# Kernel optimization log

Measured on AMD Instinct MI355X. Metric: run time of the kernel, lower is better.

Reference implementation:

```python
import jax, jax.numpy as jnp
import numpy as np

N_NODES = 50000
N_EDGES = 800000
D_IN = 64
D_OUT = 64


def setup_inputs() -> dict:
    key = jax.random.key(0)
    k1, k2, k3, k4 = jax.random.split(key, 4)
    x = jax.random.normal(k1, (N_NODES, D_IN), dtype=jnp.float32)
    edge_index = jax.random.randint(k2, (2, N_EDGES), 0, N_NODES, dtype=jnp.int64)
    W = jax.random.normal(k3, (D_IN, D_OUT), dtype=jnp.float32) * (1.0 / np.sqrt(D_IN))
    b = jax.random.normal(k4, (D_OUT,), dtype=jnp.float32) * 0.01
    return {"x": x, "edge_index": edge_index, "W": W, "b": b}


def reference(x, edge_index, W, b):
    N = x.shape[0]
    # Add self-loops (PyG GCNConv default add_self_loops=True)
    loop = jnp.arange(N, dtype=edge_index.dtype)
    src = jnp.concatenate([edge_index[0], loop])  # source j
    dst = jnp.concatenate([edge_index[1], loop])  # target i
    # Linear transform first (standard GCNConv: theta then propagate)
    xw = x @ W  # [N, D_OUT]
    # Symmetric degree normalization: deg over targets of (A + I)
    ones = jnp.ones(src.shape[0], dtype=x.dtype)
    deg = jax.ops.segment_sum(ones, dst, num_segments=N)
    dis = jnp.where(deg > 0, jax.lax.rsqrt(jnp.maximum(deg, 1.0)), 0.0)
    norm = dis[src] * dis[dst]  # [E+N]
    # Gather, weight, scatter-add
    msgs = norm[:, None] * xw[src]  # [E+N, D_OUT]
    out = jax.ops.segment_sum(msgs, dst, num_segments=N) + b
    return jax.nn.relu(out)
```

## Files before the change

### kernel.cpp

```cpp
#include <hip/hip_runtime.h>

#define N_NODES 50000
#define N_EDGES 800000
#define D 64
#define FINE_SHIFT 6
#define NBUCK 782
#define CAP 1280
#define SEGCAP 64
#define EPB 8192
#define NPART 98
#define NMM 196
#define NSTART (NBUCK + 1)

typedef _Float16 f16;
typedef __attribute__((ext_vector_type(4))) _Float16 f16x4;
typedef __attribute__((ext_vector_type(8))) _Float16 f16x8;
typedef __attribute__((ext_vector_type(4))) float f32x4;

#define SMEM_PART (2 * NBUCK * 4 + EPB * 4)
#define SMEM_MM   (64 * 72 * 2 + 256 * 72 * 2)
#define SMEM_SZ   (SMEM_MM > SMEM_PART ? SMEM_MM : SMEM_PART)

__global__ __launch_bounds__(1024) void partition_matmul(
    const int* __restrict__ src, const int* __restrict__ dst,
    unsigned int* __restrict__ binned2, int* __restrict__ starts2,
    const float* __restrict__ W, const float* __restrict__ x,
    f16* __restrict__ xwh)
{
    __shared__ __align__(16) unsigned char smem[SMEM_SZ];
    int tid = threadIdx.x;

    if (blockIdx.x >= NPART) {
        f16 (*WtH)[72]  = (f16 (*)[72])smem;
        f16 (*park)[72] = (f16 (*)[72])(smem + 64 * 72 * 2);

        for (int j = tid; j < 4096; j += 1024)
            WtH[j & 63][j >> 6] = (f16)W[j];
        __syncthreads();

        int nb = (blockIdx.x - NPART) * 256;
        int wave = tid >> 6, lane = tid & 63;
        int m = lane & 15, q = lane >> 4;

        int ar = nb + wave * 16 + m;
        if (ar >= N_NODES) ar = N_NODES - 1;
        const float4* x4 = (const float4*)x;
        size_t rb = (size_t)ar * 16;
        float4 p0 = x4[rb + q * 2];
        float4 p1 = x4[rb + q * 2 + 1];
        float4 p2 = x4[rb + 8 + q * 2];
        float4 p3 = x4[rb + 8 + q * 2 + 1];
        f16x8 a0 = { (f16)p0.x, (f16)p0.y, (f16)p0.z, (f16)p0.w,
                     (f16)p1.x, (f16)p1.y, (f16)p1.z, (f16)p1.w };
        f16x8 a1 = { (f16)p2.x, (f16)p2.y, (f16)p2.z, (f16)p2.w,
                     (f16)p3.x, (f16)p3.y, (f16)p3.z, (f16)p3.w };

        f32x4 acc[4];
        #pragma unroll
        for (int t = 0; t < 4; ++t) {
            int n0 = t * 16;
            f16x8 b0 = *(const f16x8*)&WtH[n0 + m][q * 8];
            f16x8 b1 = *(const f16x8*)&WtH[n0 + m][32 + q * 8];
            f32x4 z = { 0.f, 0.f, 0.f, 0.f };
            z = __builtin_amdgcn_mfma_f32_16x16x32_f16(a0, b0, z, 0, 0, 0);
            acc[t] = __builtin_amdgcn_mfma_f32_16x16x32_f16(a1, b1, z, 0, 0, 0);
        }

        #pragma unroll
        for (int t = 0; t < 4; ++t) {
            int n0 = t * 16;
            #pragma unroll
            for (int r = 0; r < 4; ++r)
                park[wave * 16 + q * 4 + r][n0 + m] = (f16)acc[t][r];
        }
        __syncthreads();

        for (int j = tid; j < 2048; j += 1024) {
            int row = j >> 3, seg = (j & 7) * 8;
            int n = nb + row;
            if (n < N_NODES)
                *(f16x8*)&xwh[(size_t)n * D + seg] = *(const f16x8*)&park[row][seg];
        }
        return;
    }

    int* hist            = (int*)smem;
    int* start_s         = hist + NBUCK;
    unsigned int* staged = (unsigned int*)(start_s + NBUCK);

    int eb  = blockIdx.x * EPB;
    int total = N_EDGES - eb; if (total > EPB) total = EPB;

    for (int i = tid; i < NBUCK; i += 1024) hist[i] = 0;
    __syncthreads();

    unsigned int rec[8];
    int rank[8];
    int jb = tid * 8;
    if (jb < total) {
        int4 s0 = *(const int4*)&src[eb + jb];
        int4 s1 = *(const int4*)&src[eb + jb + 4];
        int4 d0 = *(const int4*)&dst[eb + jb];
        int4 d1 = *(const int4*)&dst[eb + jb + 4];
        rec[0] = ((unsigned)d0.x << 16) | (unsigned)s0.x;
        rec[1] = ((unsigned)d0.y << 16) | (unsigned)s0.y;
        rec[2] = ((unsigned)d0.z << 16) | (unsigned)s0.z;
        rec[3] = ((unsigned)d0.w << 16) | (unsigned)s0.w;
        rec[4] = ((unsigned)d1.x << 16) | (unsigned)s1.x;
        rec[5] = ((unsigned)d1.y << 16) | (unsigned)s1.y;
        rec[6] = ((unsigned)d1.z << 16) | (unsigned)s1.z;
        rec[7] = ((unsigned)d1.w << 16) | (unsigned)s1.w;
        #pragma unroll
        for (int u = 0; u < 8; ++u)
            rank[u] = atomicAdd(&hist[rec[u] >> (16 + FINE_SHIFT)], 1);
    } else {
        #pragma unroll
        for (int u = 0; u < 8; ++u) rec[u] = 0xFFFFFFFFu;
    }
    __syncthreads();

    if (tid < 64) {
        int b0 = tid * 13;
        int v[13]; int run = 0;
        #pragma unroll
        for (int j = 0; j < 13; ++j) {
            int idx = b0 + j;
            int c = (idx < NBUCK) ? hist[idx] : 0;
            v[j] = run; run += c;
        }
        int s = run;
        #pragma unroll
        for (int off = 1; off < 64; off <<= 1) {
            int t = __shfl_up(s, off);
            if (tid >= off) s += t;
        }
        int excl = s - run;
        #pragma unroll
        for (int j = 0; j < 13; ++j) {
            int idx = b0 + j;
            if (idx < NBUCK) start_s[idx] = excl + v[j];
        }
    }
    __syncthreads();

    #pragma unroll
    for (int u = 0; u < 8; ++u) {
        unsigned int v = rec[u];
        if (v != 0xFFFFFFFFu)
            staged[start_s[v >> 22] + rank[u]] = v;
    }
    __syncthreads();

    for (int i = tid; i < total; i += 1024)
        binned2[(size_t)blockIdx.x * EPB + i] = staged[i];
    for (int i = tid; i < NBUCK; i += 1024)
        starts2[(size_t)blockIdx.x * NSTART + i] = start_s[i];
    if (tid == 0)
        starts2[(size_t)blockIdx.x * NSTART + NBUCK] = total;
}

__global__ __launch_bounds__(256) void degree_scale(
    const unsigned int* __restrict__ binned2, const int* __restrict__ starts2,
    f16* __restrict__ xwh)
{
    __shared__ int segcnt_s[NPART], segbase_s[NPART], segsrc_s[NPART];
    __shared__ int h[64];
    __shared__ int stot_s;

    int cb = blockIdx.x, tid = threadIdx.x;
    if (tid < 64) h[tid] = 0;
    if (tid < NPART) {
        int base = tid * NSTART + cb;
        int s0 = starts2[base], s1 = starts2[base + 1];
        int c = s1 - s0; if (c < 0) c = 0; if (c > SEGCAP) c = SEGCAP;
        segcnt_s[tid] = c;
        segsrc_s[tid] = tid * EPB + s0;
    }
    __syncthreads();

    if (tid < 64) {
        int v0 = segcnt_s[tid], s = v0;
        #pragma unroll
        for (int off = 1; off < 64; off <<= 1) {
            int t = __shfl_up(s, off);
            if (tid >= off) s += t;
        }
        segbase_s[tid] = s - v0;
        int T0 = __shfl(s, 63);
        int v1 = (tid < NPART - 64) ? segcnt_s[64 + tid] : 0;
        int s1 = v1;
        #pragma unroll
        for (int off = 1; off < 64; off <<= 1) {
            int t = __shfl_up(s1, off);
            if (tid >= off) s1 += t;
        }
        if (tid < NPART - 64) segbase_s[64 + tid] = T0 + s1 - v1;
        int T1 = __shfl(s1, 63);
        if (tid == 0) {
            int tot = T0 + T1; if (tot > CAP) tot = CAP;
            stot_s = tot;
        }
    }
    __syncthreads();
    if (tid < NPART) segsrc_s[tid] -= segbase_s[tid];
    __syncthreads();

    int stot = stot_s;
    for (int i = tid; i < stot; i += 256) {
        int lo = 0, hi = NPART - 1;
        #pragma unroll
        for (int it = 0; it < 7; ++it) {
            int mid = (lo + hi + 1) >> 1;
            if (segbase_s[mid] <= i) lo = mid; else hi = mid - 1;
        }
        unsigned int r = binned2[segsrc_s[lo] + i];
        atomicAdd(&h[(r >> 16) & 63], 1);
    }
    __syncthreads();

    int nb = cb * 64;
    for (int j = tid; j < 512; j += 256) {
        int row = j >> 3, seg = (j & 7) * 8;
        int n = nb + row;
        if (n < N_NODES) {
            float dn = rsqrtf((float)h[row] + 1.0f);
            f16x8 v = *(f16x8*)&xwh[(size_t)n * D + seg];
            #pragma unroll
            for (int e = 0; e < 8; ++e)
                v[e] = (f16)((float)v[e] * dn);
            *(f16x8*)&xwh[(size_t)n * D + seg] = v;
        }
    }
}

__global__ __launch_bounds__(512) void gather_out(
    const unsigned int* __restrict__ binned2, const int* __restrict__ starts2,
    const f16* __restrict__ xwh, const float* __restrict__ b,
    float* __restrict__ out)
{
    __shared__ unsigned short ssrc[CAP];
    __shared__ int h[64], off_s[64], cur[64];
    __shared__ int segcnt_s[NPART], segbase_s[NPART], segsrc_s[NPART];
    __shared__ int stot_s;

    int cb = blockIdx.x, tid = threadIdx.x;
    int wave = tid >> 6, lane = tid & 63;
    int nb = cb * 64;

    if (tid < 64) h[tid] = 0;
    if (tid < NPART) {
        int base = tid * NSTART + cb;
        int s0 = starts2[base], s1 = starts2[base + 1];
        int c = s1 - s0; if (c < 0) c = 0; if (c > SEGCAP) c = SEGCAP;
        segcnt_s[tid] = c;
        segsrc_s[tid] = tid * EPB + s0;
    }
    __syncthreads();

    if (tid < 64) {
        int v0 = segcnt_s[tid], s = v0;
        #pragma unroll
        for (int off = 1; off < 64; off <<= 1) {
            int t = __shfl_up(s, off);
            if (tid >= off) s += t;
        }
        segbase_s[tid] = s - v0;
        int T0 = __shfl(s, 63);
        int v1 = (tid < NPART - 64) ? segcnt_s[64 + tid] : 0;
        int s1 = v1;
        #pragma unroll
        for (int off = 1; off < 64; off <<= 1) {
            int t = __shfl_up(s1, off);
            if (tid >= off) s1 += t;
        }
        if (tid < NPART - 64) segbase_s[64 + tid] = T0 + s1 - v1;
        int T1 = __shfl(s1, 63);
        if (tid == 0) {
            int tot = T0 + T1; if (tot > CAP) tot = CAP;
            stot_s = tot;
        }
    }
    __syncthreads();
    if (tid < NPART) segsrc_s[tid] -= segbase_s[tid];
    __syncthreads();

    int cnt = stot_s;
    unsigned int rec[3];
    #pragma unroll
    for (int u = 0; u < 3; ++u) {
        int j = u * 512 + tid;
        if (j < cnt) {
            int lo = 0, hi = NPART - 1;
            #pragma unroll
            for (int it = 0; it < 7; ++it) {
                int mid = (lo + hi + 1) >> 1;
                if (segbase_s[mid] <= j) lo = mid; else hi = mid - 1;
            }
            rec[u] = binned2[segsrc_s[lo] + j];
            atomicAdd(&h[(rec[u] >> 16) & 63], 1);
        } else rec[u] = 0xFFFFFFFFu;
    }
    __syncthreads();

    if (tid < 64) {
        int v = h[tid], s = v;
        #pragma unroll
        for (int off = 1; off < 64; off <<= 1) {
            int t = __shfl_up(s, off);
            if (tid >= off) s += t;
        }
        off_s[tid] = s - v;
        cur[tid]   = s - v;
    }
    __syncthreads();

    #pragma unroll
    for (int u = 0; u < 3; ++u) {
        unsigned int v = rec[u];
        if (v != 0xFFFFFFFFu) {
            int p = atomicAdd(&cur[(v >> 16) & 63], 1);
            ssrc[p] = (unsigned short)(v & 0xFFFFu);
        }
    }
    __syncthreads();

    const f16x4* xw4 = (const f16x4*)xwh;
    const float4* b4p = (const float4*)b;
    float4* out4 = (float4*)out;
    int g = lane >> 4, c16 = lane & 15;

    for (int i = 0; i < 8; ++i) {
        int nl = wave * 8 + i;
        int n  = nb + nl;
        if (n >= N_NODES) break;
        int off = off_s[nl], c = h[nl];
        float dn = rsqrtf((float)c + 1.0f);

        float a0 = 0.f, a1 = 0.f, a2 = 0.f, a3 = 0.f;
        if (g == 0) {
            f16x4 sv = xw4[(size_t)n * 16 + c16];
            a0 = (float)sv.x; a1 = (float)sv.y; a2 = (float)sv.z; a3 = (float)sv.w;
        }
        int k = off + g, e = off + c;
        for (; k + 12 < e; k += 16) {
            int s0 = ssrc[k], s1 = ssrc[k + 4], s2 = ssrc[k + 8], s3 = ssrc[k + 12];
            f16x4 v0 = xw4[(size_t)s0 * 16 + c16];
            f16x4 v1 = xw4[(size_t)s1 * 16 + c16];
            f16x4 v2 = xw4[(size_t)s2 * 16 + c16];
            f16x4 v3 = xw4[(size_t)s3 * 16 + c16];
            a0 += (float)v0.x + (float)v1.x + (float)v2.x + (float)v3.x;
            a1 += (float)v0.y + (float)v1.y + (float)v2.y + (float)v3.y;
            a2 += (float)v0.z + (float)v1.z + (float)v2.z + (float)v3.z;
            a3 += (float)v0.w + (float)v1.w + (float)v2.w + (float)v3.w;
        }
        for (; k + 4 < e; k += 8) {
            int s0 = ssrc[k], s1 = ssrc[k + 4];
            f16x4 v0 = xw4[(size_t)s0 * 16 + c16];
            f16x4 v1 = xw4[(size_t)s1 * 16 + c16];
            a0 += (float)v0.x + (float)v1.x;
            a1 += (float)v0.y + (float)v1.y;
            a2 += (float)v0.z + (float)v1.z;
            a3 += (float)v0.w + (float)v1.w;
        }
        if (k < e) {
            f16x4 v = xw4[(size_t)ssrc[k] * 16 + c16];
            a0 += (float)v.x; a1 += (float)v.y; a2 += (float)v.z; a3 += (float)v.w;
        }
        a0 += __shfl_xor(a0, 32); a1 += __shfl_xor(a1, 32);
        a2 += __shfl_xor(a2, 32); a3 += __shfl_xor(a3, 32);
        a0 += __shfl_xor(a0, 16); a1 += __shfl_xor(a1, 16);
        a2 += __shfl_xor(a2, 16); a3 += __shfl_xor(a3, 16);
        if (g == 0) {
            float4 bl = b4p[c16];
            float4 r;
            r.x = fmaxf(bl.x + dn * a0, 0.f);
            r.y = fmaxf(bl.y + dn * a1, 0.f);
            r.z = fmaxf(bl.z + dn * a2, 0.f);
            r.w = fmaxf(bl.w + dn * a3, 0.f);
            out4[(size_t)n * 16 + c16] = r;
        }
    }
}

extern "C" void kernel_launch(void* const* d_in, const int* in_sizes, int n_in,
                              void* d_out, int out_size, void* d_ws, size_t ws_size,
                              hipStream_t stream) {
    const float* x  = (const float*)d_in[0];
    const int*   ei = (const int*)d_in[1];
    const float* W  = (const float*)d_in[2];
    const float* b  = (const float*)d_in[3];

    const int* src = ei;
    const int* dst = ei + N_EDGES;
    float* out = (float*)d_out;

    f16*          xwh     = (f16*)d_ws;
    unsigned int* binned2 = (unsigned int*)(xwh + (size_t)N_NODES * D);
    int*          starts2 = (int*)(binned2 + (size_t)NPART * EPB);

    partition_matmul<<<NPART + NMM, 1024, 0, stream>>>(
        src, dst, binned2, starts2, W, x, xwh);
    degree_scale<<<NBUCK, 256, 0, stream>>>(binned2, starts2, xwh);
    gather_out<<<NBUCK, 512, 0, stream>>>(binned2, starts2, xwh, b, out);
}
```

Baseline: 106.1 us.

## Fuse partition, degree-scale and gather into one persistent kernel with grid barriers

Merges the three launches into a single 256-block persistent kernel that uses atomic-counter grid barriers between the partition/matmul, degree-scaling and gather phases. Each block handles several buckets and keeps the fetched edge records in shared memory between phases, so the gather phase does not reload them from global memory. This is meant to remove launch gaps and duplicate edge-record reads. In exchange it requires all blocks to be co-resident, and the barrier counter is never reset; it depends on the workspace being pre-filled with a fixed poison value on every call.

```diff
diff --git a/kernel.cpp b/kernel.cpp
--- a/kernel.cpp
+++ b/kernel.cpp
@@ -8,377 +8,334 @@
 #define CAP 1280
 #define SEGCAP 64
 #define EPB 8192
-#define NPART 98
-#define NMM 196
+#define NPARTB 98
+#define NMMB 158
+#define NTILE 196
+#define NBLK 256
 #define NSTART (NBUCK + 1)
+#define WS_POISON 0xAAAAAAAAu
 
 typedef _Float16 f16;
 typedef __attribute__((ext_vector_type(4))) _Float16 f16x4;
 typedef __attribute__((ext_vector_type(8))) _Float16 f16x8;
 typedef __attribute__((ext_vector_type(4))) float f32x4;
 
-#define SMEM_PART (2 * NBUCK * 4 + EPB * 4)
-#define SMEM_MM   (64 * 72 * 2 + 256 * 72 * 2)
-#define SMEM_SZ   (SMEM_MM > SMEM_PART ? SMEM_MM : SMEM_PART)
-
-__global__ __launch_bounds__(1024) void partition_matmul(
+#define SMEM_SZ 46080
+
+__device__ __forceinline__ void grid_sync(unsigned int* bar, unsigned int target) {
+    __threadfence();
+    __syncthreads();
+    if (threadIdx.x == 0) {
+        atomicAdd(bar, 1u);
+        while ((unsigned)(atomicAdd(bar, 0u) - WS_POISON) < target)
+            __builtin_amdgcn_s_sleep(4);
+    }
+    __syncthreads();
+    __threadfence();
+}
+
+__global__ __launch_bounds__(1024) void gcn_mega(
     const int* __restrict__ src, const int* __restrict__ dst,
     unsigned int* __restrict__ binned2, int* __restrict__ starts2,
+    unsigned int* __restrict__ bar,
     const float* __restrict__ W, const float* __restrict__ x,
-    f16* __restrict__ xwh)
+    f16* __restrict__ xwh, const float* __restrict__ b,
+    float* __restrict__ out)
 {
     __shared__ __align__(16) unsigned char smem[SMEM_SZ];
-    int tid = threadIdx.x;
-
-    if (blockIdx.x >= NPART) {
+    const int tid = threadIdx.x;
+    const int bid = blockIdx.x;
+    const int wave = tid >> 6, lane = tid & 63;
+
+    if (bid >= NPARTB) {
         f16 (*WtH)[72]  = (f16 (*)[72])smem;
         f16 (*park)[72] = (f16 (*)[72])(smem + 64 * 72 * 2);
-
         for (int j = tid; j < 4096; j += 1024)
             WtH[j & 63][j >> 6] = (f16)W[j];
         __syncthreads();
-
-        int nb = (blockIdx.x - NPART) * 256;
-        int wave = tid >> 6, lane = tid & 63;
         int m = lane & 15, q = lane >> 4;
-
-        int ar = nb + wave * 16 + m;
-        if (ar >= N_NODES) ar = N_NODES - 1;
-        const float4* x4 = (const float4*)x;
-        size_t rb = (size_t)ar * 16;
-        float4 p0 = x4[rb + q * 2];
-        float4 p1 = x4[rb + q * 2 + 1];
-        float4 p2 = x4[rb + 8 + q * 2];
-        float4 p3 = x4[rb + 8 + q * 2 + 1];
-        f16x8 a0 = { (f16)p0.x, (f16)p0.y, (f16)p0.z, (f16)p0.w,
-                     (f16)p1.x, (f16)p1.y, (f16)p1.z, (f16)p1.w };
-        f16x8 a1 = { (f16)p2.x, (f16)p2.y, (f16)p2.z, (f16)p2.w,
-                     (f16)p3.x, (f16)p3.y, (f16)p3.z, (f16)p3.w };
-
-        f32x4 acc[4];
+        for (int k = 0; k < 2; ++k) {
+            int t = (bid - NPARTB) + NMMB * k;
+            if (t >= NTILE) break;
+            int nb = t * 256;
+            int ar = nb + wave * 16 + m;
+            if (ar >= N_NODES) ar = N_NODES - 1;
+            const float4* x4 = (const float4*)x;
+            size_t rb = (size_t)ar * 16;
+            float4 p0 = x4[rb + q * 2];
+            float4 p1 = x4[rb + q * 2 + 1];
+            float4 p2 = x4[rb + 8 + q * 2];
+            float4 p3 = x4[rb + 8 + q * 2 + 1];
+            f16x8 a0 = { (f16)p0.x, (f16)p0.y, (f16)p0.z, (f16)p0.w,
+                         (f16)p1.x, (f16)p1.y, (f16)p1.z, (f16)p1.w };
+            f16x8 a1 = { (f16)p2.x, (f16)p2.y, (f16)p2.z, (f16)p2.w,
+                         (f16)p3.x, (f16)p3.y, (f16)p3.z, (f16)p3.w };
+            f32x4 acc[4];
+            #pragma unroll
+            for (int t4 = 0; t4 < 4; ++t4) {
+                int n0 = t4 * 16;
+                f16x8 b0 = *(const f16x8*)&WtH[n0 + m][q * 8];
+                f16x8 b1 = *(const f16x8*)&WtH[n0 + m][32 + q * 8];
+                f32x4 z = { 0.f, 0.f, 0.f, 0.f };
+                z = __builtin_amdgcn_mfma_f32_16x16x32_f16(a0, b0, z, 0, 0, 0);
+                acc[t4] = __builtin_amdgcn_mfma_f32_16x16x32_f16(a1, b1, z, 0, 0, 0);
+            }
+            #pragma unroll
+            for (int t4 = 0; t4 < 4; ++t4) {
+                int n0 = t4 * 16;
+                #pragma unroll
+                for (int r = 0; r < 4; ++r)
+                    park[wave * 16 + q * 4 + r][n0 + m] = (f16)acc[t4][r];
+            }
+            __syncthreads();
+            for (int j = tid; j < 2048; j += 1024) {
+                int row = j >> 3, seg = (j & 7) * 8;
+                int n = nb + row;
+                if (n < N_NODES)
+                    *(f16x8*)&xwh[(size_t)n * D + seg] = *(const f16x8*)&park[row][seg];
+            }
+            __syncthreads();
+        }
+    } else {
+        int* hist            = (int*)smem;
+        int* start_s         = (int*)(smem + 3128);
+        unsigned int* staged = (unsigned int*)(smem + 6256);
+
+        int eb  = bid * EPB;
+        int total = N_EDGES - eb; if (total > EPB) total = EPB;
+
+        for (int i = tid; i < NBUCK; i += 1024) hist[i] = 0;
+        __syncthreads();
+
+        unsigned int rec[8];
+        int rank[8];
+        int jb = tid * 8;
+        if (jb < total) {
+            int4 s0 = *(const int4*)&src[eb + jb];
+            int4 s1 = *(const int4*)&src[eb + jb + 4];
+            int4 d0 = *(const int4*)&dst[eb + jb];
+            int4 d1 = *(const int4*)&dst[eb + jb + 4];
+            rec[0] = ((unsigned)d0.x << 16) | (unsigned)s0.x;
+            rec[1] = ((unsigned)d0.y << 16) | (unsigned)s0.y;
+            rec[2] = ((unsigned)d0.z << 16) | (unsigned)s0.z;
+            rec[3] = ((unsigned)d0.w << 16) | (unsigned)s0.w;
+            rec[4] = ((unsigned)d1.x << 16) | (unsigned)s1.x;
+            rec[5] = ((unsigned)d1.y << 16) | (unsigned)s1.y;
+            rec[6] = ((unsigned)d1.z << 16) | (unsigned)s1.z;
+            rec[7] = ((unsigned)d1.w << 16) | (unsigned)s1.w;
+            #pragma unroll
+            for (int u = 0; u < 8; ++u)
+                rank[u] = atomicAdd(&hist[rec[u] >> (16 + FINE_SHIFT)], 1);
+        } else {
+            #pragma unroll
+            for (int u = 0; u < 8; ++u) rec[u] = 0xFFFFFFFFu;
+        }
+        __syncthreads();
+
+        if (tid < 64) {
+            int b0 = tid * 13;
+            int v[13]; int run = 0;
+            #pragma unroll
+            for (int j = 0; j < 13; ++j) {
+                int idx = b0 + j;
+                int c = (idx < NBUCK) ? hist[idx] : 0;
+                v[j] = run; run += c;
+            }
+            int s = run;
+            #pragma unroll
+            for (int off = 1; off < 64; off <<= 1) {
+                int t = __shfl_up(s, off);
+                if (tid >= off) s += t;
+            }
+            int excl = s - run;
+            #pragma unroll
+            for (int j = 0; j < 13; ++j) {
+                int idx = b0 + j;
+                if (idx < NBUCK) start_s[idx] = excl + v[j];
+            }
+        }
+        __syncthreads();
+
         #pragma unroll
-        for (int t = 0; t < 4; ++t) {
-            int n0 = t * 16;
-            f16x8 b0 = *(const f16x8*)&WtH[n0 + m][q * 8];
-            f16x8 b1 = *(const f16x8*)&WtH[n0 + m][32 + q * 8];
-            f32x4 z = { 0.f, 0.f, 0.f, 0.f };
-            z = __builtin_amdgcn_mfma_f32_16x16x32_f16(a0, b0, z, 0, 0, 0);
-            acc[t] = __builtin_amdgcn_mfma_f32_16x16x32_f16(a1, b1, z, 0, 0, 0);
-        }
-
-        #pragma unroll
-        for (int t = 0; t < 4; ++t) {
-            int n0 = t * 16;
-            #pragma unroll
-            for (int r = 0; r < 4; ++r)
-                park[wave * 16 + q * 4 + r][n0 + m] = (f16)acc[t][r];
-        }
-        __syncthreads();
-
-        for (int j = tid; j < 2048; j += 1024) {
+        for (int u = 0; u < 8; ++u) {
+            unsigned int v = rec[u];
+            if (v != 0xFFFFFFFFu)
+                staged[start_s[v >> 22] + rank[u]] = v;
+        }
+        __syncthreads();
+
+        for (int i = tid; i < total; i += 1024)
+            binned2[(size_t)bid * EPB + i] = staged[i];
+        for (int i = tid; i < NBUCK; i += 1024)
+            starts2[(size_t)bid * NSTART + i] = start_s[i];
+        if (tid == 0)
+            starts2[(size_t)bid * NSTART + NBUCK] = total;
+    }
+
+    grid_sync(bar, NBLK);
+
+    unsigned int*  srec    = (unsigned int*)smem;
+    int*           hists   = (int*)(smem + 20480);
+    int*           segcnt  = (int*)(smem + 21504);
+    int*           segbase = (int*)(smem + 22016);
+    int*           segsrc  = (int*)(smem + 22528);
+    int*           scnt    = (int*)(smem + 23040);
+    unsigned short* ssrc   = (unsigned short*)(smem + 23056);
+    int*           off_s   = (int*)(smem + 25616);
+    int*           cur     = (int*)(smem + 25872);
+
+    for (int qq = 0; qq < 4; ++qq) {
+        int cb = bid + qq * NBLK;
+        if (cb >= NBUCK) break;
+        if (tid < 64) hists[qq * 64 + tid] = 0;
+        int s0r = 0;
+        if (tid < NPARTB) {
+            int base = tid * NSTART + cb;
+            s0r = starts2[base];
+            int s1 = starts2[base + 1];
+            int c = s1 - s0r; if (c < 0) c = 0; if (c > SEGCAP) c = SEGCAP;
+            segcnt[tid] = c;
+        }
+        __syncthreads();
+        if (tid < 64) {
+            int b2 = tid * 2;
+            int c0 = (b2     < NPARTB) ? segcnt[b2]     : 0;
+            int c1 = (b2 + 1 < NPARTB) ? segcnt[b2 + 1] : 0;
+            int run = c0 + c1;
+            int s = run;
+            #pragma unroll
+            for (int off = 1; off < 64; off <<= 1) {
+                int t = __shfl_up(s, off);
+                if (tid >= off) s += t;
+            }
+            int excl = s - run;
+            segbase[b2]     = excl;
+            segbase[b2 + 1] = excl + c0;
+            if (tid == 63) {
+                int tot = excl + run; if (tot > CAP) tot = CAP;
+                scnt[qq] = tot;
+            }
+        }
+        __syncthreads();
+        if (tid < NPARTB) segsrc[tid] = tid * EPB + s0r - segbase[tid * 2 == tid * 2 ? tid : tid];
+        __syncthreads();
+        if (tid < NPARTB) segsrc[tid] = tid * EPB + s0r - segbase[tid];
+        __syncthreads();
+
+        int stot = scnt[qq];
+        for (int i = tid; i < stot; i += 1024) {
+            int lo = 0, hi = 127;
+            #pragma unroll
+            for (int it = 0; it < 7; ++it) {
+                int mid = (lo + hi + 1) >> 1;
+                if (segbase[mid] <= i) lo = mid; else hi = mid - 1;
+            }
+            unsigned int r = binned2[segsrc[lo] + i];
+            srec[qq * CAP + i] = r;
+            atomicAdd(&hists[qq * 64 + ((r >> 16) & 63)], 1);
+        }
+        __syncthreads();
+
+        int nb = cb * 64;
+        for (int j = tid; j < 512; j += 1024) {
             int row = j >> 3, seg = (j & 7) * 8;
             int n = nb + row;
-            if (n < N_NODES)
-                *(f16x8*)&xwh[(size_t)n * D + seg] = *(const f16x8*)&park[row][seg];
-        }
-        return;
+            if (n < N_NODES) {
+                float dn = rsqrtf((float)hists[qq * 64 + row] + 1.0f);
+                f16x8 v = *(f16x8*)&xwh[(size_t)n * D + seg];
+                #pragma unroll
+                for (int e = 0; e < 8; ++e)
+                    v[e] = (f16)((float)v[e] * dn);
+                *(f16x8*)&xwh[(size_t)n * D + seg] = v;
+            }
+        }
+        __syncthreads();
     }
 
-    int* hist            = (int*)smem;
-    int* start_s         = hist + NBUCK;
-    unsigned int* staged = (unsigned int*)(start_s + NBUCK);
-
-    int eb  = blockIdx.x * EPB;
-    int total = N_EDGES - eb; if (total > EPB) total = EPB;
-
-    for (int i = tid; i < NBUCK; i += 1024) hist[i] = 0;
-    __syncthreads();
-
-    unsigned int rec[8];
-    int rank[8];
-    int jb = tid * 8;
-    if (jb < total) {
-        int4 s0 = *(const int4*)&src[eb + jb];
-        int4 s1 = *(const int4*)&src[eb + jb + 4];
-        int4 d0 = *(const int4*)&dst[eb + jb];
-        int4 d1 = *(const int4*)&dst[eb + jb + 4];
-        rec[0] = ((unsigned)d0.x << 16) | (unsigned)s0.x;
-        rec[1] = ((unsigned)d0.y << 16) | (unsigned)s0.y;
-        rec[2] = ((unsigned)d0.z << 16) | (unsigned)s0.z;
-        rec[3] = ((unsigned)d0.w << 16) | (unsigned)s0.w;
-        rec[4] = ((unsigned)d1.x << 16) | (unsigned)s1.x;
-        rec[5] = ((unsigned)d1.y << 16) | (unsigned)s1.y;
-        rec[6] = ((unsigned)d1.z << 16) | (unsigned)s1.z;
-        rec[7] = ((unsigned)d1.w << 16) | (unsigned)s1.w;
-        #pragma unroll
-        for (int u = 0; u < 8; ++u)
-            rank[u] = atomicAdd(&hist[rec[u] >> (16 + FINE_SHIFT)], 1);
-    } else {
-        #pragma unroll
-        for (int u = 0; u < 8; ++u) rec[u] = 0xFFFFFFFFu;
-    }
-    __syncthreads();
-
-    if (tid < 64) {
-        int b0 = tid * 13;
-        int v[13]; int run = 0;
-        #pragma unroll
-        for (int j = 0; j < 13; ++j) {
-            int idx = b0 + j;
-            int c = (idx < NBUCK) ? hist[idx] : 0;
-            v[j] = run; run += c;
-        }
-        int s = run;
-        #pragma unroll
-        for (int off = 1; off < 64; off <<= 1) {
-            int t = __shfl_up(s, off);
-            if (tid >= off) s += t;
-        }
-        int excl = s - run;
-        #pragma unroll
-        for (int j = 0; j < 13; ++j) {
-            int idx = b0 + j;
-            if (idx < NBUCK) start_s[idx] = excl + v[j];
-        }
-    }
-    __syncthreads();
-
-    #pragma unroll
-    for (int u = 0; u < 8; ++u) {
-        unsigned int v = rec[u];
-        if (v != 0xFFFFFFFFu)
-            staged[start_s[v >> 22] + rank[u]] = v;
-    }
-    __syncthreads();
-
-    for (int i = tid; i < total; i += 1024)
-        binned2[(size_t)blockIdx.x * EPB + i] = staged[i];
-    for (int i = tid; i < NBUCK; i += 1024)
-        starts2[(size_t)blockIdx.x * NSTART + i] = start_s[i];
-    if (tid == 0)
-        starts2[(size_t)blockIdx.x * NSTART + NBUCK] = total;
-}
-
-__global__ __launch_bounds__(256) void degree_scale(
-    const unsigned int* __restrict__ binned2, const int* __restrict__ starts2,
-    f16* __restrict__ xwh)
-{
-    __shared__ int segcnt_s[NPART], segbase_s[NPART], segsrc_s[NPART];
-    __shared__ int h[64];
-    __shared__ int stot_s;
-
-    int cb = blockIdx.x, tid = threadIdx.x;
-    if (tid < 64) h[tid] = 0;
-    if (tid < NPART) {
-        int base = tid * NSTART + cb;
-        int s0 = starts2[base], s1 = starts2[base + 1];
-        int c = s1 - s0; if (c < 0) c = 0; if (c > SEGCAP) c = SEGCAP;
-        segcnt_s[tid] = c;
-        segsrc_s[tid] = tid * EPB + s0;
-    }
-    __syncthreads();
-
-    if (tid < 64) {
-        int v0 = segcnt_s[tid], s = v0;
-        #pragma unroll
-        for (int off = 1; off < 64; off <<= 1) {
-            int t = __shfl_up(s, off);
-            if (tid >= off) s += t;
-        }
-        segbase_s[tid] = s - v0;
-        int T0 = __shfl(s, 63);
-        int v1 = (tid < NPART - 64) ? segcnt_s[64 + tid] : 0;
-        int s1 = v1;
-        #pragma unroll
-        for (int off = 1; off < 64; off <<= 1) {
-            int t = __shfl_up(s1, off);
-            if (tid >= off) s1 += t;
-        }
-        if (tid < NPART - 64) segbase_s[64 + tid] = T0 + s1 - v1;
-        int T1 = __shfl(s1, 63);
-        if (tid == 0) {
-            int tot = T0 + T1; if (tot > CAP) tot = CAP;
-            stot_s = tot;
-        }
-    }
-    __syncthreads();
-    if (tid < NPART) segsrc_s[tid] -= segbase_s[tid];
-    __syncthreads();
-
-    int stot = stot_s;
-    for (int i = tid; i < stot; i += 256) {
-        int lo = 0, hi = NPART - 1;
-        #pragma unroll
-        for (int it = 0; it < 7; ++it) {
-            int mid = (lo + hi + 1) >> 1;
-            if (segbase_s[mid] <= i) lo = mid; else hi = mid - 1;
-        }
-        unsigned int r = binned2[segsrc_s[lo] + i];
-        atomicAdd(&h[(r >> 16) & 63], 1);
-    }
-    __syncthreads();
-
-    int nb = cb * 64;
-    for (int j = tid; j < 512; j += 256) {
-        int row = j >> 3, seg = (j & 7) * 8;
-        int n = nb + row;
-        if (n < N_NODES) {
-            float dn = rsqrtf((float)h[row] + 1.0f);
-            f16x8 v = *(f16x8*)&xwh[(size_t)n * D + seg];
-            #pragma unroll
-            for (int e = 0; e < 8; ++e)
-                v[e] = (f16)((float)v[e] * dn);
-            *(f16x8*)&xwh[(size_t)n * D + seg] = v;
-        }
-    }
-}
-
-__global__ __launch_bounds__(512) void gather_out(
-    const unsigned int* __restrict__ binned2, const int* __restrict__ starts2,
-    const f16* __restrict__ xwh, const float* __restrict__ b,
-    float* __restrict__ out)
-{
-    __shared__ unsigned short ssrc[CAP];
-    __shared__ int h[64], off_s[64], cur[64];
-    __shared__ int segcnt_s[NPART], segbase_s[NPART], segsrc_s[NPART];
-    __shared__ int stot_s;
-
-    int cb = blockIdx.x, tid = threadIdx.x;
-    int wave = tid >> 6, lane = tid & 63;
-    int nb = cb * 64;
-
-    if (tid < 64) h[tid] = 0;
-    if (tid < NPART) {
-        int base = tid * NSTART + cb;
-        int s0 = starts2[base], s1 = starts2[base + 1];
-        int c = s1 - s0; if (c < 0) c = 0; if (c > SEGCAP) c = SEGCAP;
-        segcnt_s[tid] = c;
-        segsrc_s[tid] = tid * EPB + s0;
-    }
-    __syncthreads();
-
-    if (tid < 64) {
-        int v0 = segcnt_s[tid], s = v0;
-        #pragma unroll
-        for (int off = 1; off < 64; off <<= 1) {
-            int t = __shfl_up(s, off);
-            if (tid >= off) s += t;
-        }
-        segbase_s[tid] = s - v0;
-        int T0 = __shfl(s, 63);
-        int v1 = (tid < NPART - 64) ? segcnt_s[64 + tid] : 0;
-        int s1 = v1;
-        #pragma unroll
-        for (int off = 1; off < 64; off <<= 1) {
-            int t = __shfl_up(s1, off);
-            if (tid >= off) s1 += t;
-        }
-        if (tid < NPART - 64) segbase_s[64 + tid] = T0 + s1 - v1;
-        int T1 = __shfl(s1, 63);
-        if (tid == 0) {
-            int tot = T0 + T1; if (tot > CAP) tot = CAP;
-            stot_s = tot;
-        }
-    }
-    __syncthreads();
-    if (tid < NPART) segsrc_s[tid] -= segbase_s[tid];
-    __syncthreads();
-
-    int cnt = stot_s;
-    unsigned int rec[3];
-    #pragma unroll
-    for (int u = 0; u < 3; ++u) {
-        int j = u * 512 + tid;
-        if (j < cnt) {
-            int lo = 0, hi = NPART - 1;
-            #pragma unroll
-            for (int it = 0; it < 7; ++it) {
-                int mid = (lo + hi + 1) >> 1;
-                if (segbase_s[mid] <= j) lo = mid; else hi = mid - 1;
-            }
-            rec[u] = binned2[segsrc_s[lo] + j];
-            atomicAdd(&h[(rec[u] >> 16) & 63], 1);
-        } else rec[u] = 0xFFFFFFFFu;
-    }
-    __syncthreads();
-
-    if (tid < 64) {
-        int v = h[tid], s = v;
-        #pragma unroll
-        for (int off = 1; off < 64; off <<= 1) {
-            int t = __shfl_up(s, off);
-            if (tid >= off) s += t;
-        }
-        off_s[tid] = s - v;
-        cur[tid]   = s - v;
-    }
-    __syncthreads();
-
-    #pragma unroll
-    for (int u = 0; u < 3; ++u) {
-        unsigned int v = rec[u];
-        if (v != 0xFFFFFFFFu) {
-            int p = atomicAdd(&cur[(v >> 16) & 63], 1);
-            ssrc[p] = (unsigned short)(v & 0xFFFFu);
-        }
-    }
-    __syncthreads();
+    grid_sync(bar, 2 * NBLK);
 
     const f16x4* xw4 = (const f16x4*)xwh;
     const float4* b4p = (const float4*)b;
     float4* out4 = (float4*)out;
     int g = lane >> 4, c16 = lane & 15;
 
-    for (int i = 0; i < 8; ++i) {
-        int nl = wave * 8 + i;
-        int n  = nb + nl;
-        if (n >= N_NODES) break;
-        int off = off_s[nl], c = h[nl];
-        float dn = rsqrtf((float)c + 1.0f);
-
-        float a0 = 0.f, a1 = 0.f, a2 = 0.f, a3 = 0.f;
-        if (g == 0) {
-            f16x4 sv = xw4[(size_t)n * 16 + c16];
-            a0 = (float)sv.x; a1 = (float)sv.y; a2 = (float)sv.z; a3 = (float)sv.w;
-        }
-        int k = off + g, e = off + c;
-        for (; k + 12 < e; k += 16) {
-            int s0 = ssrc[k], s1 = ssrc[k + 4], s2 = ssrc[k + 8], s3 = ssrc[k + 12];
-            f16x4 v0 = xw4[(size_t)s0 * 16 + c16];
-            f16x4 v1 = xw4[(size_t)s1 * 16 + c16];
-            f16x4 v2 = xw4[(size_t)s2 * 16 + c16];
-            f16x4 v3 = xw4[(size_t)s3 * 16 + c16];
-            a0 += (float)v0.x + (float)v1.x + (float)v2.x + (float)v3.x;
-            a1 += (float)v0.y + (float)v1.y + (float)v2.y + (float)v3.y;
-            a2 += (float)v0.z + (float)v1.z + (float)v2.z + (float)v3.z;
-            a3 += (float)v0.w + (float)v1.w + (float)v2.w + (float)v3.w;
-        }
-        for (; k + 4 < e; k += 8) {
-            int s0 = ssrc[k], s1 = ssrc[k + 4];
-            f16x4 v0 = xw4[(size_t)s0 * 16 + c16];
-            f16x4 v1 = xw4[(size_t)s1 * 16 + c16];
-            a0 += (float)v0.x + (float)v1.x;
-            a1 += (float)v0.y + (float)v1.y;
-            a2 += (float)v0.z + (float)v1.z;
-            a3 += (float)v0.w + (float)v1.w;
-        }
-        if (k < e) {
-            f16x4 v = xw4[(size_t)ssrc[k] * 16 + c16];
-            a0 += (float)v.x; a1 += (float)v.y; a2 += (float)v.z; a3 += (float)v.w;
-        }
-        a0 += __shfl_xor(a0, 32); a1 += __shfl_xor(a1, 32);
-        a2 += __shfl_xor(a2, 32); a3 += __shfl_xor(a3, 32);
-        a0 += __shfl_xor(a0, 16); a1 += __shfl_xor(a1, 16);
-        a2 += __shfl_xor(a2, 16); a3 += __shfl_xor(a3, 16);
-        if (g == 0) {
-            float4 bl = b4p[c16];
-            float4 r;
-            r.x = fmaxf(bl.x + dn * a0, 0.f);
-            r.y = fmaxf(bl.y + dn * a1, 0.f);
-            r.z = fmaxf(bl.z + dn * a2, 0.f);
-            r.w = fmaxf(bl.w + dn * a3, 0.f);
-            out4[(size_t)n * 16 + c16] = r;
-        }
+    for (int qq = 0; qq < 4; ++qq) {
+        int cb = bid + qq * NBLK;
+        if (cb >= NBUCK) break;
+        int nb = cb * 64;
+        int stot = scnt[qq];
+        int* h = &hists[qq * 64];
+
+        if (tid < 64) {
+            int v = h[tid], s = v;
+            #pragma unroll
+            for (int off = 1; off < 64; off <<= 1) {
+                int t = __shfl_up(s, off);
+                if (tid >= off) s += t;
+            }
+            off_s[tid] = s - v;
+            cur[tid]   = s - v;
+        }
+        __syncthreads();
+        for (int i = tid; i < stot; i += 1024) {
+            unsigned int v = srec[qq * CAP + i];
+            int p = atomicAdd(&cur[(v >> 16) & 63], 1);
+            ssrc[p] = (unsigned short)(v & 0xFFFFu);
+        }
+        __syncthreads();
+
+        for (int i = 0; i < 4; ++i) {
+            int nl = wave * 4 + i;
+            int n  = nb + nl;
+            if (n >= N_NODES) break;
+            int off = off_s[nl], c = h[nl];
+            float dn = rsqrtf((float)c + 1.0f);
+
+            float a0 = 0.f, a1 = 0.f, a2 = 0.f, a3 = 0.f;
+            if (g == 0) {
+                f16x4 sv = xw4[(size_t)n * 16 + c16];
+                a0 = (float)sv.x; a1 = (float)sv.y; a2 = (float)sv.z; a3 = (float)sv.w;
+            }
+            int k = off + g, e = off + c;
+            for (; k + 12 < e; k += 16) {
+                int s0 = ssrc[k], s1 = ssrc[k + 4], s2 = ssrc[k + 8], s3 = ssrc[k + 12];
+                f16x4 v0 = xw4[(size_t)s0 * 16 + c16];
+                f16x4 v1 = xw4[(size_t)s1 * 16 + c16];
+                f16x4 v2 = xw4[(size_t)s2 * 16 + c16];
+                f16x4 v3 = xw4[(size_t)s3 * 16 + c16];
+                a0 += (float)v0.x + (float)v1.x + (float)v2.x + (float)v3.x;
+                a1 += (float)v0.y + (float)v1.y + (float)v2.y + (float)v3.y;
+                a2 += (float)v0.z + (float)v1.z + (float)v2.z + (float)v3.z;
+                a3 += (float)v0.w + (float)v1.w + (float)v2.w + (float)v3.w;
+            }
+            for (; k + 4 < e; k += 8) {
+                int s0 = ssrc[k], s1 = ssrc[k + 4];
+                f16x4 v0 = xw4[(size_t)s0 * 16 + c16];
+                f16x4 v1 = xw4[(size_t)s1 * 16 + c16];
+                a0 += (float)v0.x + (float)v1.x;
+                a1 += (float)v0.y + (float)v1.y;
+                a2 += (float)v0.z + (float)v1.z;
+                a3 += (float)v0.w + (float)v1.w;
+            }
+            if (k < e) {
+                f16x4 v = xw4[(size_t)ssrc[k] * 16 + c16];
+                a0 += (float)v.x; a1 += (float)v.y; a2 += (float)v.z; a3 += (float)v.w;
+            }
+            a0 += __shfl_xor(a0, 32); a1 += __shfl_xor(a1, 32);
+            a2 += __shfl_xor(a2, 32); a3 += __shfl_xor(a3, 32);
+            a0 += __shfl_xor(a0, 16); a1 += __shfl_xor(a1, 16);
+            a2 += __shfl_xor(a2, 16); a3 += __shfl_xor(a3, 16);
+            if (g == 0) {
+                float4 bl = b4p[c16];
+                float4 r;
+                r.x = fmaxf(bl.x + dn * a0, 0.f);
+                r.y = fmaxf(bl.y + dn * a1, 0.f);
+                r.z = fmaxf(bl.z + dn * a2, 0.f);
+                r.w = fmaxf(bl.w + dn * a3, 0.f);
+                out4[(size_t)n * 16 + c16] = r;
+            }
+        }
+        __syncthreads();
     }
 }
 
@@ -396,10 +353,9 @@
 
     f16*          xwh     = (f16*)d_ws;
     unsigned int* binned2 = (unsigned int*)(xwh + (size_t)N_NODES * D);
-    int*          starts2 = (int*)(binned2 + (size_t)NPART * EPB);
-
-    partition_matmul<<<NPART + NMM, 1024, 0, stream>>>(
-        src, dst, binned2, starts2, W, x, xwh);
-    degree_scale<<<NBUCK, 256, 0, stream>>>(binned2, starts2, xwh);
-    gather_out<<<NBUCK, 512, 0, stream>>>(binned2, starts2, xwh, b, out);
+    int*          starts2 = (int*)(binned2 + (size_t)NPARTB * EPB);
+    unsigned int* bar     = (unsigned int*)(starts2 + (size_t)NPARTB * NSTART);
+
+    gcn_mega<<<NBLK, 1024, 0, stream>>>(
+        src, dst, binned2, starts2, bar, W, x, xwh, b, out);
 }
```

Result: slower. 403.8 us (+280.4%).
